# Performance work log

Hardware: AMD Instinct MI355X
Metric: run time of the kernel (lower is better)

Reference implementation:

```python
import jax, jax.numpy as jnp
import numpy as np

EPS = 1e-6

def l2norm(x):
    # kernel.normalize: L2-normalize along the last (head_dim) axis
    return x * jax.lax.rsqrt(jnp.sum(x * x, axis=-1, keepdims=True) + EPS)

def setup_inputs() -> dict:
    key = jax.random.key(0)
    kq, kk, kv = jax.random.split(key, 3)
    B, H, S, D = 2, 12, 2048, 64
    Q = jax.random.normal(kq, (B, H, S, D), dtype=jnp.float32)
    K = jax.random.normal(kk, (B, H, S, D), dtype=jnp.float32)
    V = jax.random.normal(kv, (B, H, S, D), dtype=jnp.float32)
    mask = jnp.ones((B, S), dtype=jnp.int32)
    return {"Q": Q, "K": K, "V": V, "mask": mask, "hashcode_len": 9}

def reference(Q, K, V, mask, hashcode_len):
    # YOSO expectation kernel (num_hash_f < 0 path):
    #   Qn, Kn = L2-normalize(Q), L2-normalize(K)
    #   W[i,j] = (1 - arccos(<q_i, k_j>)/pi) ** hashcode_len   (collision prob of LSH)
    #   X = W @ V with key/query masking, then L2-normalize X.
    Qn = l2norm(Q)                                 # [B,H,S,D]
    Kn = l2norm(K)
    m = mask.astype(Q.dtype)                       # [B,S]
    sim = jnp.einsum('bhsd,bhtd->bhst', Qn, Kn)    # cosine similarities in [-1,1]
    sim = jnp.clip(sim, -1.0 + EPS, 1.0 - EPS)
    w = (1.0 - jnp.arccos(sim) / jnp.pi) ** hashcode_len   # [B,H,S,S]
    w = w * m[:, None, None, :]                    # mask keys
    X = jnp.einsum('bhst,bhtd->bhsd', w, V)        # [B,H,S,D]
    X = X * m[:, None, :, None]                    # mask queries
    X = l2norm(X)                                  # kernel.normalize(X)
    return X
```

## Files before the change

kernel.cpp:

```cpp
#include <hip/hip_runtime.h>
#include <hip/hip_bf16.h>
#include <hip/hip_fp16.h>

typedef short bf16x8 __attribute__((ext_vector_type(8)));
typedef _Float16 h8 __attribute__((ext_vector_type(8)));
typedef _Float16 h2v __attribute__((ext_vector_type(2)));
typedef __fp16 fp16x2 __attribute__((ext_vector_type(2)));
typedef float f32x16 __attribute__((ext_vector_type(16)));
typedef unsigned int uint32;

#define S 2048
#define D 64
#define NBH 24

#define GLOAD16(g, l) __builtin_amdgcn_global_load_lds(                      \
    (const __attribute__((address_space(1))) unsigned int*)(g),              \
    (__attribute__((address_space(3))) unsigned int*)(l), 16, 0, 0)

__device__ __forceinline__ int cvtpk_bf16(float lo, float hi) {
    int r;
    asm("v_cvt_pk_bf16_f32 %0, %1, %2" : "=v"(r) : "v"(lo), "v"(hi));
    return r;
}

__global__ __launch_bounds__(256) void prep(const float* __restrict__ Q,
                                            const float* __restrict__ K,
                                            const float* __restrict__ V,
                                            const int* __restrict__ mask,
                                            __hip_bfloat16* __restrict__ Qn,
                                            __hip_bfloat16* __restrict__ Kn,
                                            __half* __restrict__ Vt) {
    __shared__ float tile[64][65];
    const int NBQK = 2 * NBH * S / 16;
    int blk = blockIdx.x;
    int t = threadIdx.x;
    if (blk < NBQK) {
        int l16 = t & 15;
        int row = blk * 16 + (t >> 4);
        int half = row >= NBH * S;
        const float* in = half ? K : Q;
        __hip_bfloat16* out = half ? Kn : Qn;
        row -= half * NBH * S;
        float4 x = *(const float4*)(in + (size_t)row * 64 + l16 * 4);
        float ss = x.x * x.x + x.y * x.y + x.z * x.z + x.w * x.w;
        #pragma unroll
        for (int m = 1; m <= 8; m <<= 1) ss += __shfl_xor(ss, m, 64);
        float sc = rsqrtf(ss + 1e-6f);
        int2 pk = { cvtpk_bf16(x.x * sc, x.y * sc), cvtpk_bf16(x.z * sc, x.w * sc) };
        *(int2*)(out + (size_t)row * 64 + l16 * 4) = pk;
        return;
    }
    blk -= NBQK;
    int bh = blk >> 5;
    int b  = bh / 12;
    int s0 = (blk & 31) << 6;
    #pragma unroll
    for (int i = 0; i < 16; ++i) {
        int idx = i * 256 + t;
        int sl = idx >> 6, d = idx & 63;
        float mv = (float)mask[b * S + s0 + sl];
        tile[sl][d] = V[(size_t)bh * S * D + (size_t)(s0 + sl) * D + d] * mv;
    }
    __syncthreads();
    #pragma unroll
    for (int i = 0; i < 16; ++i) {
        int idx = i * 256 + t;
        int d = idx >> 6, sl = idx & 63;
        Vt[(size_t)bh * S * D + (size_t)d * S + s0 + sl] = __float2half(tile[sl][d]);
    }
}

template<int SPLITS>
__global__ __launch_bounds__(512) void yoso_main(const __hip_bfloat16* __restrict__ Qn,
                                                 const __hip_bfloat16* __restrict__ Kn,
                                                 const __half* __restrict__ Vt,
                                                 const int* __restrict__ mask,
                                                 const int* __restrict__ hlen_ptr,
                                                 void* __restrict__ outp) {
    __shared__ char lds[2][16384];

    const int QT = 16;
    const int blk = blockIdx.x;
    const int bh  = blk / (QT * SPLITS);
    const int rr  = blk % (QT * SPLITS);
    const int q0  = (rr / SPLITS) << 7;
    const int kq  = rr % SPLITS;
    const int kbase = kq * (S / SPLITS);
    const int NTt   = S / SPLITS / 64;

    const int b    = bh / 12;
    const int t    = threadIdx.x;
    const int w    = t >> 6;
    const int lane = t & 63;
    const int h    = lane >> 5;
    const int c31  = lane & 31;
    const int qh   = w >> 1;
    const int kh   = w & 1;
    const int hcode = hlen_ptr[0];
    const size_t head = (size_t)bh * S * D;

    const int s_  = lane & 7;
    const int r3l = lane >> 3;
    const int e1  = s_ ^ r3l ^ (w & 7);
    const int u1  = e1 ^ ((e1 & 1) << 2);
    const int kgo1 = (8 * w + r3l) * 128 + u1 * 16;
    const int vgo1 = (8 * w + r3l) * 4096 + u1 * 16;
    const char* Kg = (const char*)(Kn + head);
    const char* Vg = (const char*)(Vt + head);

    char* ldsc = &lds[0][0];
    int koffs[4], voffs[2][2];
    {
        int krow = kh * 32 + c31;
        int kb3  = (krow & 7) ^ (krow >> 3) ^ (h << 2) ^ h;
        #pragma unroll
        for (int kd = 0; kd < 4; ++kd)
            koffs[kd] = krow * 128 + (((2 * kd) ^ kb3)) * 16;
        int vb3 = (c31 & 7) ^ (c31 >> 3) ^ (h << 2) ^ h ^ (kh << 2);
        #pragma unroll
        for (int kb2 = 0; kb2 < 2; ++kb2) {
            voffs[kb2][0] = c31 * 128        + (((kb2 << 1) ^ vb3)) * 16     + 8192;
            voffs[kb2][1] = (32 + c31) * 128 + (((kb2 << 1) ^ vb3 ^ 4)) * 16 + 8192;
        }
    }

    bf16x8 qf[4];
    {
        const __hip_bfloat16* qp = Qn + head + (size_t)(q0 + qh * 32 + c31) * D + h * 8;
        qf[0] = *(const bf16x8*)(qp);
        qf[1] = *(const bf16x8*)(qp + 16);
        qf[2] = *(const bf16x8*)(qp + 32);
        qf[3] = *(const bf16x8*)(qp + 48);
    }
    asm volatile("" :: "v"(qf[0]), "v"(qf[1]), "v"(qf[2]), "v"(qf[3]));

    const f32x16 z16 = {0,0,0,0,0,0,0,0,0,0,0,0,0,0,0,0};
    f32x16 xacc0 = z16, xacc1 = z16;

    const bool  p9 = (hcode == 9);
    const float hf = (float)hcode;

    const h2v one2  = {(_Float16)1.0f,  (_Float16)1.0f};
    const h2v half2 = {(_Float16)0.5f,  (_Float16)0.5f};
    const h2v zero2 = {(_Float16)0.0f,  (_Float16)0.0f};
    const h2v q3c = {(_Float16)-0.00596128f, (_Float16)-0.00596128f};
    const h2v q2c = {(_Float16)-0.00575336f, (_Float16)-0.00575336f};
    const h2v q1c = {(_Float16)-0.03812704f, (_Float16)-0.03812704f};
    const h2v q0c = {(_Float16)-0.4501324f,  (_Float16)-0.4501324f};

    auto STAGE = [&](int base, int k0) {
        const char* kb = Kg + (size_t)k0 * 128;
        const char* vb = Vg + (size_t)k0 * 2;
        char* Kl = ldsc + base;
        char* Vl = Kl + 8192;
        GLOAD16(kb + kgo1, Kl + w * 1024);
        GLOAD16(vb + vgo1, Vl + w * 1024);
    };

    auto XFgen = [&](float s) -> float {
        float z  = fmaxf(1.0f - fabsf(s), 0.0f);
        float qp = ((0.00596128f * z + 0.00575336f) * z + 0.03812704f) * z + 0.4501324f;
        float tp = 0.5f - __builtin_amdgcn_sqrtf(z) * qp;
        float x  = 0.5f + __builtin_copysignf(tp, s);
        return __builtin_amdgcn_exp2f(hf * __builtin_amdgcn_logf(x));
    };

    auto COMPUTE = [&](int bufbase) {
        const char* base = ldsc + bufbase;
        __builtin_amdgcn_s_setprio(1);
        f32x16 sacc = __builtin_amdgcn_mfma_f32_32x32x16_bf16(
            *(const bf16x8*)(base + koffs[0]), qf[0], z16, 0, 0, 0);
        #pragma unroll
        for (int kd = 1; kd < 4; ++kd)
            sacc = __builtin_amdgcn_mfma_f32_32x32x16_bf16(
                *(const bf16x8*)(base + koffs[kd]), qf[kd], sacc, 0, 0, 0);
        __builtin_amdgcn_s_setprio(0);

        int u_[8];
        union HU { h2v v; fp16x2 p; uint32 u; };
        if (p9) {
            #pragma unroll
            for (int i = 0; i < 8; ++i) {
                HU cv; cv.p = __builtin_amdgcn_cvt_pkrtz(sacc[2 * i], sacc[2 * i + 1]);
                uint32 spb = cv.u;
                HU za; za.u = spb & 0x7FFF7FFFu;
                h2v z = one2 - za.v;
                z = __builtin_elementwise_max(z, zero2);
                h2v rt = __builtin_elementwise_sqrt(z);
                h2v q = q3c * z + q2c;
                q = q * z + q1c;
                q = q * z + q0c;
                HU tb; tb.v = q * rt + half2;
                HU xb; xb.u = (tb.u & 0x7FFF7FFFu) | (spb & 0x80008000u);
                h2v x = xb.v + half2;
                h2v x2 = x * x;
                h2v x4 = x2 * x2;
                h2v x8 = x4 * x4;
                HU wr; wr.v = x8 * x;
                u_[i] = (int)wr.u;
            }
        } else {
            #pragma unroll
            for (int i = 0; i < 8; ++i) {
                HU cv;
                cv.p = __builtin_amdgcn_cvt_pkrtz(XFgen(sacc[2 * i]),
                                                  XFgen(sacc[2 * i + 1]));
                u_[i] = (int)cv.u;
            }
        }
        asm("v_permlane32_swap_b32 %0, %1" : "+v"(u_[0]), "+v"(u_[2]));
        asm("v_permlane32_swap_b32 %0, %1" : "+v"(u_[1]), "+v"(u_[3]));
        asm("v_permlane32_swap_b32 %0, %1" : "+v"(u_[4]), "+v"(u_[6]));
        asm("v_permlane32_swap_b32 %0, %1" : "+v"(u_[5]), "+v"(u_[7]));
        union { int i[4]; h8 v; } f0, f1;
        f0.i[0] = u_[0]; f0.i[1] = u_[1]; f0.i[2] = u_[2]; f0.i[3] = u_[3];
        f1.i[0] = u_[4]; f1.i[1] = u_[5]; f1.i[2] = u_[6]; f1.i[3] = u_[7];

        h8 vf00 = *(const h8*)(base + voffs[0][0]);
        h8 vf01 = *(const h8*)(base + voffs[0][1]);
        h8 vf10 = *(const h8*)(base + voffs[1][0]);
        h8 vf11 = *(const h8*)(base + voffs[1][1]);
        __builtin_amdgcn_s_setprio(1);
        xacc0 = __builtin_amdgcn_mfma_f32_32x32x16_f16(f0.v, vf00, xacc0, 0, 0, 0);
        xacc1 = __builtin_amdgcn_mfma_f32_32x32x16_f16(f0.v, vf01, xacc1, 0, 0, 0);
        xacc0 = __builtin_amdgcn_mfma_f32_32x32x16_f16(f1.v, vf10, xacc0, 0, 0, 0);
        xacc1 = __builtin_amdgcn_mfma_f32_32x32x16_f16(f1.v, vf11, xacc1, 0, 0, 0);
        __builtin_amdgcn_s_setprio(0);
    };

    STAGE(0, kbase);
    for (int t2 = 0; t2 < NTt; ++t2) {
        asm volatile("s_waitcnt vmcnt(0)" ::: "memory");
        __builtin_amdgcn_s_barrier();
        if (t2 + 1 < NTt) STAGE(((t2 + 1) & 1) * 16384, kbase + (t2 + 1) * 64);
        COMPUTE((t2 & 1) * 16384);
    }

    __syncthreads();
    float* red = (float*)ldsc;
    if (kh == 1) {
        #pragma unroll
        for (int r = 0; r < 16; ++r) {
            int q = (r & 3) + 8 * (r >> 2) + 4 * h;
            red[(qh * 32 + q) * 64 + c31]      = xacc0[r];
            red[(qh * 32 + q) * 64 + 32 + c31] = xacc1[r];
        }
    }
    __syncthreads();
    if (kh == 0) {
        #pragma unroll
        for (int r = 0; r < 16; ++r) {
            int q  = (r & 3) + 8 * (r >> 2) + 4 * h;
            int qg = q0 + qh * 32 + q;
            float x0 = xacc0[r] + red[(qh * 32 + q) * 64 + c31];
            float x1 = xacc1[r] + red[(qh * 32 + q) * 64 + 32 + c31];
            if (SPLITS > 1) {
                __half* pp = (__half*)outp + ((size_t)(kq * NBH + bh) * S + qg) * D;
                pp[c31]      = __float2half(x0);
                pp[32 + c31] = __float2half(x1);
            } else {
                float mq = (float)mask[b * S + qg];
                x0 *= mq; x1 *= mq;
                float ss = x0 * x0 + x1 * x1;
                #pragma unroll
                for (int m = 1; m <= 16; m <<= 1) ss += __shfl_xor(ss, m, 64);
                float sc = rsqrtf(ss + 1e-6f);
                float* op = (float*)outp + ((size_t)bh * S + qg) * D;
                op[c31]      = x0 * sc;
                op[32 + c31] = x1 * sc;
            }
        }
    }
}

template<int SPLITS>
__global__ __launch_bounds__(256) void combine_norm(const __half* __restrict__ P,
                                                    const int* __restrict__ mask,
                                                    float* __restrict__ out) {
    int t = threadIdx.x;
    int l16 = t & 15;
    size_t row = (size_t)blockIdx.x * 16 + (t >> 4);
    size_t i = row * 64 + l16 * 4;
    float x0 = 0.f, x1 = 0.f, x2 = 0.f, x3 = 0.f;
    #pragma unroll
    for (int k = 0; k < SPLITS; ++k) {
        const __half2* p2 = (const __half2*)(P + (size_t)k * NBH * S * D + i);
        __half2 ab = p2[0], cd = p2[1];
        x0 += __low2float(ab); x1 += __high2float(ab);
        x2 += __low2float(cd); x3 += __high2float(cd);
    }
    int bh = (int)(row >> 11);
    int sidx = (int)(row & 2047);
    int b = bh / 12;
    float mq = (float)mask[b * S + sidx];
    x0 *= mq; x1 *= mq; x2 *= mq; x3 *= mq;
    float ss = x0 * x0 + x1 * x1 + x2 * x2 + x3 * x3;
    #pragma unroll
    for (int m = 1; m <= 8; m <<= 1) ss += __shfl_xor(ss, m, 64);
    float sc = rsqrtf(ss + 1e-6f);
    float4 o = { x0 * sc, x1 * sc, x2 * sc, x3 * sc };
    *(float4*)(out + i) = o;
}

extern "C" void kernel_launch(void* const* d_in, const int* in_sizes, int n_in,
                              void* d_out, int out_size, void* d_ws, size_t ws_size,
                              hipStream_t stream) {
    const float* Q    = (const float*)d_in[0];
    const float* K    = (const float*)d_in[1];
    const float* V    = (const float*)d_in[2];
    const int*   mask = (const int*)d_in[3];
    const int*   hlen = (const int*)d_in[4];
    float*       out  = (float*)d_out;

    __hip_bfloat16* Qn = (__hip_bfloat16*)d_ws;
    __hip_bfloat16* Kn = Qn + (size_t)NBH * S * D;
    __half*         Vt = (__half*)(Kn + (size_t)NBH * S * D);
    __half* Pbuf = (__half*)((char*)d_ws + 3ull * NBH * S * D * 2);

    const size_t base_b = 3ull * NBH * S * D * 2;
    const size_t part_h = (size_t)NBH * S * D * 2;

    prep<<<2 * NBH * S / 16 + NBH * 32, 256, 0, stream>>>(Q, K, V, mask, Qn, Kn, Vt);
    if (ws_size >= base_b + 4 * part_h) {
        yoso_main<4><<<NBH * 16 * 4, 512, 0, stream>>>(Qn, Kn, Vt, mask, hlen, Pbuf);
        combine_norm<4><<<NBH * S / 16, 256, 0, stream>>>(Pbuf, mask, out);
    } else if (ws_size >= base_b + 2 * part_h) {
        yoso_main<2><<<NBH * 16 * 2, 512, 0, stream>>>(Qn, Kn, Vt, mask, hlen, Pbuf);
        combine_norm<2><<<NBH * S / 16, 256, 0, stream>>>(Pbuf, mask, out);
    } else {
        yoso_main<1><<<NBH * 16, 512, 0, stream>>>(Qn, Kn, Vt, mask, hlen, out);
    }
}
```

Before: 71.23 us.

## Double block size to 256 queries and stage two key tiles per barrier

Each block now has 1024 threads and covers 256 query rows instead of 128, so every staged K/V tile is shared by twice as many query rows. The first eight waves load K and the other eight load V. LDS grows to four 16KB buffers, and two 64-key tiles are prefetched and computed per barrier, which halves the number of barriers and waitcnts. The cost is 64KB of LDS per block, fewer blocks (768 in the default path) and lower occupancy. Unseen code such as the qf loads and the reduction must also handle the 16 waves correctly (qh now spans 0..7).

```diff
diff --git a/kernel.cpp b/kernel.cpp
--- a/kernel.cpp
+++ b/kernel.cpp
@@ -71,19 +71,19 @@
 }
 
 template<int SPLITS>
-__global__ __launch_bounds__(512) void yoso_main(const __hip_bfloat16* __restrict__ Qn,
-                                                 const __hip_bfloat16* __restrict__ Kn,
-                                                 const __half* __restrict__ Vt,
-                                                 const int* __restrict__ mask,
-                                                 const int* __restrict__ hlen_ptr,
-                                                 void* __restrict__ outp) {
-    __shared__ char lds[2][16384];
-
-    const int QT = 16;
+__global__ __launch_bounds__(1024) void yoso_main(const __hip_bfloat16* __restrict__ Qn,
+                                                  const __hip_bfloat16* __restrict__ Kn,
+                                                  const __half* __restrict__ Vt,
+                                                  const int* __restrict__ mask,
+                                                  const int* __restrict__ hlen_ptr,
+                                                  void* __restrict__ outp) {
+    __shared__ char lds[4][16384];
+
+    const int QT = 8;
     const int blk = blockIdx.x;
     const int bh  = blk / (QT * SPLITS);
     const int rr  = blk % (QT * SPLITS);
-    const int q0  = (rr / SPLITS) << 7;
+    const int q0  = (rr / SPLITS) << 8;
     const int kq  = rr % SPLITS;
     const int kbase = kq * (S / SPLITS);
     const int NTt   = S / SPLITS / 64;
@@ -99,12 +99,14 @@
     const int hcode = hlen_ptr[0];
     const size_t head = (size_t)bh * S * D;
 
-    const int s_  = lane & 7;
-    const int r3l = lane >> 3;
-    const int e1  = s_ ^ r3l ^ (w & 7);
-    const int u1  = e1 ^ ((e1 & 1) << 2);
-    const int kgo1 = (8 * w + r3l) * 128 + u1 * 16;
-    const int vgo1 = (8 * w + r3l) * 4096 + u1 * 16;
+    const int  krole = (w < 8);
+    const int  tloc  = krole ? t : (t - 512);
+    const int  trow  = tloc >> 3;
+    const int  tslot = t & 7;
+    const int  e1    = tslot ^ (trow & 7) ^ (trow >> 3);
+    const int  u1    = e1 ^ ((e1 & 1) << 2);
+    const int  goff  = krole ? (trow * 128 + u1 * 16) : (trow * 4096 + u1 * 16);
+    const int  dstoff = krole ? (w * 1024) : (8192 + (w - 8) * 1024);
     const char* Kg = (const char*)(Kn + head);
     const char* Vg = (const char*)(Vt + head);
 
@@ -148,13 +150,10 @@
     const h2v q1c = {(_Float16)-0.03812704f, (_Float16)-0.03812704f};
     const h2v q0c = {(_Float16)-0.4501324f,  (_Float16)-0.4501324f};
 
-    auto STAGE = [&](int base, int k0) {
-        const char* kb = Kg + (size_t)k0 * 128;
-        const char* vb = Vg + (size_t)k0 * 2;
-        char* Kl = ldsc + base;
-        char* Vl = Kl + 8192;
-        GLOAD16(kb + kgo1, Kl + w * 1024);
-        GLOAD16(vb + vgo1, Vl + w * 1024);
+    auto STAGE = [&](int buf, int k0) {
+        const char* src = (krole ? (Kg + (size_t)k0 * 128) : (Vg + (size_t)k0 * 2))
+                        + goff;
+        GLOAD16(src, ldsc + buf * 16384 + dstoff);
     };
 
     auto XFgen = [&](float s) -> float {
@@ -165,8 +164,8 @@
         return __builtin_amdgcn_exp2f(hf * __builtin_amdgcn_logf(x));
     };
 
-    auto COMPUTE = [&](int bufbase) {
-        const char* base = ldsc + bufbase;
+    auto COMPUTE = [&](int buf) {
+        const char* base = ldsc + buf * 16384;
         __builtin_amdgcn_s_setprio(1);
         f32x16 sacc = __builtin_amdgcn_mfma_f32_32x32x16_bf16(
             *(const bf16x8*)(base + koffs[0]), qf[0], z16, 0, 0, 0);
@@ -229,11 +228,16 @@
     };
 
     STAGE(0, kbase);
-    for (int t2 = 0; t2 < NTt; ++t2) {
+    STAGE(1, kbase + 64);
+    for (int t2 = 0; t2 < NTt; t2 += 2) {
         asm volatile("s_waitcnt vmcnt(0)" ::: "memory");
         __builtin_amdgcn_s_barrier();
-        if (t2 + 1 < NTt) STAGE(((t2 + 1) & 1) * 16384, kbase + (t2 + 1) * 64);
-        COMPUTE((t2 & 1) * 16384);
+        if (t2 + 2 < NTt) {
+            STAGE((t2 + 2) & 3, kbase + (t2 + 2) * 64);
+            STAGE((t2 + 3) & 3, kbase + (t2 + 3) * 64);
+        }
+        COMPUTE(t2 & 3);
+        COMPUTE((t2 + 1) & 3);
     }
 
     __syncthreads();
@@ -322,12 +326,12 @@
 
     prep<<<2 * NBH * S / 16 + NBH * 32, 256, 0, stream>>>(Q, K, V, mask, Qn, Kn, Vt);
     if (ws_size >= base_b + 4 * part_h) {
-        yoso_main<4><<<NBH * 16 * 4, 512, 0, stream>>>(Qn, Kn, Vt, mask, hlen, Pbuf);
+        yoso_main<4><<<NBH * 8 * 4, 1024, 0, stream>>>(Qn, Kn, Vt, mask, hlen, Pbuf);
         combine_norm<4><<<NBH * S / 16, 256, 0, stream>>>(Pbuf, mask, out);
     } else if (ws_size >= base_b + 2 * part_h) {
-        yoso_main<2><<<NBH * 16 * 2, 512, 0, stream>>>(Qn, Kn, Vt, mask, hlen, Pbuf);
+        yoso_main<2><<<NBH * 8 * 2, 1024, 0, stream>>>(Qn, Kn, Vt, mask, hlen, Pbuf);
         combine_norm<2><<<NBH * S / 16, 256, 0, stream>>>(Pbuf, mask, out);
     } else {
-        yoso_main<1><<<NBH * 16, 512, 0, stream>>>(Qn, Kn, Vt, mask, hlen, out);
-    }
-}
+        yoso_main<1><<<NBH * 8, 1024, 0, stream>>>(Qn, Kn, Vt, mask, hlen, out);
+    }
+}
```

Result: slower. 77.83 us (+9.3%).
